# Kernel optimization log

Measured on AMD Instinct MI355X. Metric: run time of the kernel, lower is better.

The kernel has to match this reference:

```python
import jax, jax.numpy as jnp
import numpy as np

GROUP_SIZE = 32
QMIN, QMAX = -128, 127  # int8 activation range


def setup_inputs() -> dict:
    key = jax.random.key(0)
    k1, k2, k3, k4 = jax.random.split(key, 4)
    B, S, IN, OUT = 4, 2048, 4096, 11008
    G = IN // GROUP_SIZE
    x = jax.random.normal(k1, (B, S, IN), dtype=jnp.float32)
    # unpacked uint4 stored as int8, values in [0, 16)
    weight = jax.random.randint(k2, (OUT, IN), 0, 16, dtype=jnp.int8)
    scales = jax.random.uniform(k3, (OUT, G), minval=0.005, maxval=0.02, dtype=jnp.float32)
    zeros = jax.random.randint(k4, (OUT, G), 0, 16).astype(jnp.float32)
    return {"input": x, "weight": weight, "scales": scales, "zeros": zeros}


def reference(input, weight, scales, zeros):
    OUT, IN = weight.shape
    G = IN // GROUP_SIZE
    # groupwise dequant of int4 weights: w_fp = (q - zero) * scale per group
    w = weight.astype(jnp.float32).reshape(OUT, G, GROUP_SIZE)
    w_dq = ((w - zeros[:, :, None]) * scales[:, :, None]).reshape(OUT, IN)
    # dynamic per-token symmetric int8 quantization of the activation
    amax = jnp.max(jnp.abs(input), axis=-1, keepdims=True)  # [B,S,1]
    a_scale = jnp.maximum(amax, 1e-12) / 127.0
    q_act = jnp.clip(jnp.round(input / a_scale), QMIN, QMAX)
    x_dq = q_act * a_scale  # fake-quantized activation, same math as int8 dot * scales
    # fused dequant-matmul: [B,S,IN] x [OUT,IN] -> [B,S,OUT]
    return jnp.einsum('bsi,oi->bso', x_dq, w_dq)
```

## Files before the change

kernel.cpp:

```cpp
#include <hip/hip_runtime.h>
#include <hip/hip_bf16.h>
#include <stdint.h>

#define M_TOK 8192
#define K_IN  4096
#define N_OUT 11008
#define G_CNT 128
#define BM 128
#define BN 256
#define TILES_M 64
#define TILES_N 43

typedef __attribute__((ext_vector_type(4)))  int   int4v;
typedef __attribute__((ext_vector_type(16))) int   int16v;
typedef __attribute__((ext_vector_type(4)))  float floatx4;

__device__ __forceinline__ void gld16(const void* g, void* lds) {
  __builtin_amdgcn_global_load_lds(
      (const __attribute__((address_space(1))) unsigned int*)g,
      (__attribute__((address_space(3))) unsigned int*)lds,
      16, 0, 0);
}

__device__ __forceinline__ int swz(int r) { return (r & 3) ^ ((r >> 2) & 1); }

__global__ void detect_kernel(const int* __restrict__ w, int* __restrict__ flag) {
  int bad = 0;
  int t = threadIdx.x;
  for (int i = t; i < 4096; i += 64) {
    int v = w[i];
    bad |= (v < 0) | (v > 15);
  }
  bad = __any(bad);
  if (t == 0) *flag = bad ? 1 : 0;
}

__global__ __launch_bounds__(256) void wdq8_kernel(
    const int* __restrict__ w, const float* __restrict__ scales,
    const float* __restrict__ zeros, signed char* __restrict__ w8,
    float* __restrict__ wrsc, const int* __restrict__ flag) {
  int n = blockIdx.x;
  int t = threadIdx.x;
  int k0 = t << 4;
  int g  = k0 >> 5;
  float s = scales[(size_t)n * G_CNT + g];
  float z = zeros[(size_t)n * G_CNT + g];
  float wf[16];
  if (*flag == 0) {
    const int4* p = (const int4*)(w + (size_t)n * K_IN + k0);
#pragma unroll
    for (int i = 0; i < 4; ++i) {
      int4 a = p[i];
      wf[4 * i + 0] = ((float)a.x - z) * s;
      wf[4 * i + 1] = ((float)a.y - z) * s;
      wf[4 * i + 2] = ((float)a.z - z) * s;
      wf[4 * i + 3] = ((float)a.w - z) * s;
    }
  } else {
    const unsigned char* wb = (const unsigned char*)w;
    uint4 u = *(const uint4*)(wb + (size_t)n * K_IN + k0);
    unsigned int uu[4] = {u.x, u.y, u.z, u.w};
#pragma unroll
    for (int i = 0; i < 4; ++i)
#pragma unroll
      for (int b = 0; b < 4; ++b)
        wf[4 * i + b] = ((float)((uu[i] >> (8 * b)) & 0xFFu) - z) * s;
  }
  float mx = 0.f;
#pragma unroll
  for (int i = 0; i < 16; ++i) mx = fmaxf(mx, fabsf(wf[i]));
#pragma unroll
  for (int off = 32; off > 0; off >>= 1)
    mx = fmaxf(mx, __shfl_xor(mx, off, 64));
  __shared__ float sm[4];
  if ((t & 63) == 0) sm[t >> 6] = mx;
  __syncthreads();
  mx = fmaxf(fmaxf(sm[0], sm[1]), fmaxf(sm[2], sm[3]));
  mx = fmaxf(mx, 1e-20f);
  if (t == 0) wrsc[n] = mx / 127.f;
  float inv = 127.f / mx;
  unsigned int ob[4];
#pragma unroll
  for (int i = 0; i < 4; ++i) {
    unsigned int v = 0;
#pragma unroll
    for (int b = 0; b < 4; ++b) {
      int q = (int)rintf(wf[4 * i + b] * inv);
      q = q > 127 ? 127 : (q < -127 ? -127 : q);
      v |= ((unsigned int)(q & 0xFF)) << (8 * b);
    }
    ob[i] = v;
  }
  *(uint4*)(w8 + (size_t)n * K_IN + k0) = make_uint4(ob[0], ob[1], ob[2], ob[3]);
}

__global__ __launch_bounds__(256) void act8_kernel(
    const float* __restrict__ x, signed char* __restrict__ aq,
    float* __restrict__ ascale) {
  int row = blockIdx.x;
  const float4* xr = (const float4*)(x + (size_t)row * K_IN);
  int t = threadIdx.x;
  float4 v[4];
  float am = 0.f;
#pragma unroll
  for (int i = 0; i < 4; ++i) {
    v[i] = xr[i * 256 + t];
    am = fmaxf(am, fmaxf(fmaxf(fabsf(v[i].x), fabsf(v[i].y)),
                         fmaxf(fabsf(v[i].z), fabsf(v[i].w))));
  }
#pragma unroll
  for (int off = 32; off > 0; off >>= 1)
    am = fmaxf(am, __shfl_xor(am, off, 64));
  __shared__ float sm[4];
  if ((t & 63) == 0) sm[t >> 6] = am;
  __syncthreads();
  am = fmaxf(fmaxf(sm[0], sm[1]), fmaxf(sm[2], sm[3]));
  float as_ = fmaxf(am, 1e-12f) / 127.f;
  if (t == 0) ascale[row] = as_;
  int* op = (int*)(aq + (size_t)row * K_IN);
#pragma unroll
  for (int i = 0; i < 4; ++i) {
    float qf[4] = {v[i].x, v[i].y, v[i].z, v[i].w};
    unsigned int pk = 0;
#pragma unroll
    for (int b = 0; b < 4; ++b) {
      float q = fminf(fmaxf(rintf(qf[b] / as_), -128.f), 127.f);
      pk |= ((unsigned int)((int)q & 0xFF)) << (8 * b);
    }
    op[i * 256 + t] = (int)pk;
  }
}

__global__ __launch_bounds__(256, 2) void gemm_i8_kernel(
    const signed char* __restrict__ A8,
    const signed char* __restrict__ W8,
    const float* __restrict__ Ascale,
    const float* __restrict__ Wrsc,
    float* __restrict__ C) {
  __shared__ __attribute__((aligned(16))) signed char lA[BM * 64];
  __shared__ __attribute__((aligned(16))) signed char lB[BN * 64];

  int bx = blockIdx.x;
  int band = bx / (8 * TILES_N);
  int rem  = bx % (8 * TILES_N);
  int tm = band * 8 + (rem & 7);
  int tn = rem >> 3;
  int m0 = tm * BM, n0 = tn * BN;

  int t = threadIdx.x;
  int lane = t & 63;
  int w = t >> 6;
  int wm = (w >> 1) * 64, wn = (w & 1) * 128;
  int half = lane >> 5, r31 = lane & 31;

  int lrow = lane >> 2;
  int lchunk = lane & 3;
  const signed char* pA[2];
  const signed char* pB[4];
#pragma unroll
  for (int r = 0; r < 2; ++r) {
    int grow = w * 32 + r * 16 + lrow;
    int scol = (lchunk ^ swz(grow)) << 4;
    pA[r] = A8 + (size_t)(m0 + grow) * K_IN + scol;
  }
#pragma unroll
  for (int r = 0; r < 4; ++r) {
    int grow = w * 64 + r * 16 + lrow;
    int scol = (lchunk ^ swz(grow)) << 4;
    pB[r] = W8 + (size_t)(n0 + grow) * K_IN + scol;
  }

  int aoff[2][2], boff[4][2];
#pragma unroll
  for (int i = 0; i < 2; ++i) {
    int R = wm + i * 32 + r31;
    int sw = swz(R);
#pragma unroll
    for (int ks = 0; ks < 2; ++ks)
      aoff[i][ks] = R * 64 + (((ks * 2 + half) ^ sw) << 4);
  }
#pragma unroll
  for (int j = 0; j < 4; ++j) {
    int R = wn + j * 32 + r31;
    int sw = swz(R);
#pragma unroll
    for (int ks = 0; ks < 2; ++ks)
      boff[j][ks] = R * 64 + (((ks * 2 + half) ^ sw) << 4);
  }

  int16v acc[2][4];
#pragma unroll
  for (int i = 0; i < 2; ++i)
#pragma unroll
    for (int j = 0; j < 4; ++j)
#pragma unroll
      for (int e = 0; e < 16; ++e) acc[i][j][e] = 0;

  char* lAb = (char*)lA;
  char* lBb = (char*)lB;

  for (int k0 = 0; k0 < K_IN; k0 += 64) {
#pragma unroll
    for (int r = 0; r < 2; ++r)
      gld16(pA[r], lAb + (w * 32 + r * 16) * 64);
#pragma unroll
    for (int r = 0; r < 4; ++r)
      gld16(pB[r], lBb + (w * 64 + r * 16) * 64);
#pragma unroll
    for (int r = 0; r < 2; ++r) pA[r] += 64;
#pragma unroll
    for (int r = 0; r < 4; ++r) pB[r] += 64;
    __syncthreads();

#pragma unroll
    for (int ks = 0; ks < 2; ++ks) {
      int4v af[2], bf[4];
#pragma unroll
      for (int i = 0; i < 2; ++i) af[i] = *(const int4v*)(lAb + aoff[i][ks]);
#pragma unroll
      for (int j = 0; j < 4; ++j) bf[j] = *(const int4v*)(lBb + boff[j][ks]);
#pragma unroll
      for (int i = 0; i < 2; ++i)
#pragma unroll
        for (int j = 0; j < 4; ++j)
          acc[i][j] = __builtin_amdgcn_mfma_i32_32x32x32_i8(af[i], bf[j], acc[i][j], 0, 0, 0);
    }
    __syncthreads();
  }

  float wsv[4];
#pragma unroll
  for (int j = 0; j < 4; ++j) wsv[j] = Wrsc[n0 + wn + j * 32 + r31];
#pragma unroll
  for (int i = 0; i < 2; ++i) {
#pragma unroll
    for (int rh = 0; rh < 4; ++rh) {
#pragma unroll
      for (int rl = 0; rl < 4; ++rl) {
        int rg = rh * 4 + rl;
        int gm = m0 + wm + i * 32 + rl + 8 * rh + 4 * half;
        float s = Ascale[gm];
        float* crow = C + (size_t)gm * N_OUT + n0 + wn + r31;
#pragma unroll
        for (int j = 0; j < 4; ++j)
          crow[j * 32] = s * wsv[j] * (float)acc[i][j][rg];
      }
    }
  }
}

extern "C" void kernel_launch(void* const* d_in, const int* in_sizes, int n_in,
                              void* d_out, int out_size, void* d_ws, size_t ws_size,
                              hipStream_t stream) {
  const float* x      = (const float*)d_in[0];
  const int*   wraw   = (const int*)d_in[1];
  const float* scales = (const float*)d_in[2];
  const float* zeros  = (const float*)d_in[3];
  float* out = (float*)d_out;

  char* ws = (char*)d_ws;
  signed char* W8 = (signed char*)ws;
  signed char* A8 = (signed char*)(ws + (size_t)N_OUT * K_IN);
  float* Wrsc   = (float*)(ws + (size_t)N_OUT * K_IN + (size_t)M_TOK * K_IN);
  float* Ascale = Wrsc + N_OUT;
  int* flag = (int*)(Ascale + M_TOK);

  detect_kernel<<<1, 64, 0, stream>>>(wraw, flag);
  wdq8_kernel<<<N_OUT, 256, 0, stream>>>(wraw, scales, zeros, W8, Wrsc, flag);
  act8_kernel<<<M_TOK, 256, 0, stream>>>(x, A8, Ascale);
  gemm_i8_kernel<<<TILES_M * TILES_N, 256, 0, stream>>>(A8, W8, Ascale, Wrsc, out);
}
```

Measured before the change: 1.005 ms.

## Triple-buffer LDS tiles in int8 GEMM with async prefetch and MFMA priority

Replaces the single-buffered LDS load/compute loop with a three-stage ring buffer. Each k-step now issues the global-to-LDS loads two steps ahead and waits only on the older loads with partial vmcnt. It also raises wave priority around the MFMA block so compute gets issued ahead of memory work. This aims to hide global load latency behind MFMA work, at the cost of triple the LDS per block (72KB), which may lower occupancy below the two blocks per CU requested in the launch bounds.

```diff
diff --git a/kernel.cpp b/kernel.cpp
--- a/kernel.cpp
+++ b/kernel.cpp
@@ -10,6 +10,8 @@
 #define BN 256
 #define TILES_M 64
 #define TILES_N 43
+#define KT_CNT 64
+#define BUF_BYTES 24576
 
 typedef __attribute__((ext_vector_type(4)))  int   int4v;
 typedef __attribute__((ext_vector_type(16))) int   int16v;
@@ -137,8 +139,7 @@
     const float* __restrict__ Ascale,
     const float* __restrict__ Wrsc,
     float* __restrict__ C) {
-  __shared__ __attribute__((aligned(16))) signed char lA[BM * 64];
-  __shared__ __attribute__((aligned(16))) signed char lB[BN * 64];
+  __shared__ __attribute__((aligned(16))) signed char ldsbuf[3 * BUF_BYTES];
 
   int bx = blockIdx.x;
   int band = bx / (8 * TILES_N);
@@ -196,10 +197,9 @@
 #pragma unroll
       for (int e = 0; e < 16; ++e) acc[i][j][e] = 0;
 
-  char* lAb = (char*)lA;
-  char* lBb = (char*)lB;
-
-  for (int k0 = 0; k0 < K_IN; k0 += 64) {
+  auto STAGE = [&](int bo) {
+    char* lAb = (char*)ldsbuf + bo;
+    char* lBb = lAb + 8192;
 #pragma unroll
     for (int r = 0; r < 2; ++r)
       gld16(pA[r], lAb + (w * 32 + r * 16) * 64);
@@ -210,8 +210,11 @@
     for (int r = 0; r < 2; ++r) pA[r] += 64;
 #pragma unroll
     for (int r = 0; r < 4; ++r) pB[r] += 64;
-    __syncthreads();
-
+  };
+
+  auto COMPUTE = [&](int bo) {
+    const char* lAb = (const char*)ldsbuf + bo;
+    const char* lBb = lAb + 8192;
 #pragma unroll
     for (int ks = 0; ks < 2; ++ks) {
       int4v af[2], bf[4];
@@ -219,14 +222,44 @@
       for (int i = 0; i < 2; ++i) af[i] = *(const int4v*)(lAb + aoff[i][ks]);
 #pragma unroll
       for (int j = 0; j < 4; ++j) bf[j] = *(const int4v*)(lBb + boff[j][ks]);
+      __builtin_amdgcn_s_setprio(1);
 #pragma unroll
       for (int i = 0; i < 2; ++i)
 #pragma unroll
         for (int j = 0; j < 4; ++j)
           acc[i][j] = __builtin_amdgcn_mfma_i32_32x32x32_i8(af[i], bf[j], acc[i][j], 0, 0, 0);
-    }
-    __syncthreads();
-  }
+      __builtin_amdgcn_s_setprio(0);
+    }
+  };
+
+  STAGE(0);
+  STAGE(BUF_BYTES);
+
+  int curo = 0;
+  int stgo = 2 * BUF_BYTES;
+
+  for (int kt = 0; kt < KT_CNT - 2; ++kt) {
+    STAGE(stgo);
+    asm volatile("s_waitcnt vmcnt(12)" ::: "memory");
+    __builtin_amdgcn_s_barrier();
+    asm volatile("" ::: "memory");
+    COMPUTE(curo);
+    asm volatile("" ::: "memory");
+    __builtin_amdgcn_s_barrier();
+    asm volatile("" ::: "memory");
+    curo = (curo == 2 * BUF_BYTES) ? 0 : curo + BUF_BYTES;
+    stgo = (stgo == 2 * BUF_BYTES) ? 0 : stgo + BUF_BYTES;
+  }
+  asm volatile("s_waitcnt vmcnt(6)" ::: "memory");
+  __builtin_amdgcn_s_barrier();
+  asm volatile("" ::: "memory");
+  COMPUTE(curo);
+  curo = (curo == 2 * BUF_BYTES) ? 0 : curo + BUF_BYTES;
+  asm volatile("" ::: "memory");
+  asm volatile("s_waitcnt vmcnt(0)" ::: "memory");
+  __builtin_amdgcn_s_barrier();
+  asm volatile("" ::: "memory");
+  COMPUTE(curo);
 
   float wsv[4];
 #pragma unroll
```

Result: no change. 992.0 us (-1.3%).

## Enlarge GEMM tile to 256x256 with triple-buffered LDS pipeline

Applied to the files above, without the earlier changes.

Grows the int8 GEMM block tile from 128x256 to 256x256 with 512 threads (8 waves, each computing 128x64), and replaces the load-sync-compute loop with a triple-buffered LDS pipeline. Global-to-LDS loads for later k-tiles are interleaved with MFMA quads under fine-grained barriers and s_setprio. The aim is to hide global load latency and raise data reuse per byte loaded. The cost is 96KB of LDS per block plus many barriers per k-tile, which may limit occupancy to one block per CU despite the launch bound of 2.

```diff
diff --git a/kernel.cpp b/kernel.cpp
--- a/kernel.cpp
+++ b/kernel.cpp
@@ -6,14 +6,16 @@
 #define K_IN  4096
 #define N_OUT 11008
 #define G_CNT 128
-#define BM 128
+#define BM 256
 #define BN 256
-#define TILES_M 64
+#define TILES_M 32
 #define TILES_N 43
+#define KT_CNT 64
+#define ABYTES 16384
+#define BUF_BYTES 32768
 
 typedef __attribute__((ext_vector_type(4)))  int   int4v;
 typedef __attribute__((ext_vector_type(16))) int   int16v;
-typedef __attribute__((ext_vector_type(4)))  float floatx4;
 
 __device__ __forceinline__ void gld16(const void* g, void* lds) {
   __builtin_amdgcn_global_load_lds(
@@ -131,14 +133,13 @@
   }
 }
 
-__global__ __launch_bounds__(256, 2) void gemm_i8_kernel(
+__global__ __launch_bounds__(512, 2) void gemm_i8_kernel(
     const signed char* __restrict__ A8,
     const signed char* __restrict__ W8,
     const float* __restrict__ Ascale,
     const float* __restrict__ Wrsc,
     float* __restrict__ C) {
-  __shared__ __attribute__((aligned(16))) signed char lA[BM * 64];
-  __shared__ __attribute__((aligned(16))) signed char lB[BN * 64];
+  __shared__ __attribute__((aligned(16))) signed char ldsbuf[3 * BUF_BYTES];
 
   int bx = blockIdx.x;
   int band = bx / (8 * TILES_N);
@@ -150,29 +151,27 @@
   int t = threadIdx.x;
   int lane = t & 63;
   int w = t >> 6;
-  int wm = (w >> 1) * 64, wn = (w & 1) * 128;
+  int wm = (w >> 2) * 128;
+  int wn = (w & 3) * 64;
   int half = lane >> 5, r31 = lane & 31;
 
   int lrow = lane >> 2;
   int lchunk = lane & 3;
   const signed char* pA[2];
-  const signed char* pB[4];
+  const signed char* pB[2];
 #pragma unroll
   for (int r = 0; r < 2; ++r) {
     int grow = w * 32 + r * 16 + lrow;
     int scol = (lchunk ^ swz(grow)) << 4;
     pA[r] = A8 + (size_t)(m0 + grow) * K_IN + scol;
-  }
-#pragma unroll
-  for (int r = 0; r < 4; ++r) {
-    int grow = w * 64 + r * 16 + lrow;
-    int scol = (lchunk ^ swz(grow)) << 4;
     pB[r] = W8 + (size_t)(n0 + grow) * K_IN + scol;
   }
-
-  int aoff[2][2], boff[4][2];
-#pragma unroll
-  for (int i = 0; i < 2; ++i) {
+  int sArow0 = (w * 32) * 64;
+  int sArow1 = (w * 32 + 16) * 64;
+
+  int aoff[4][2], boff[2][2];
+#pragma unroll
+  for (int i = 0; i < 4; ++i) {
     int R = wm + i * 32 + r31;
     int sw = swz(R);
 #pragma unroll
@@ -180,7 +179,7 @@
       aoff[i][ks] = R * 64 + (((ks * 2 + half) ^ sw) << 4);
   }
 #pragma unroll
-  for (int j = 0; j < 4; ++j) {
+  for (int j = 0; j < 2; ++j) {
     int R = wn + j * 32 + r31;
     int sw = swz(R);
 #pragma unroll
@@ -188,51 +187,98 @@
       boff[j][ks] = R * 64 + (((ks * 2 + half) ^ sw) << 4);
   }
 
-  int16v acc[2][4];
-#pragma unroll
-  for (int i = 0; i < 2; ++i)
-#pragma unroll
-    for (int j = 0; j < 4; ++j)
+  int16v acc[4][2];
+#pragma unroll
+  for (int i = 0; i < 4; ++i)
+#pragma unroll
+    for (int j = 0; j < 2; ++j)
 #pragma unroll
       for (int e = 0; e < 16; ++e) acc[i][j][e] = 0;
 
-  char* lAb = (char*)lA;
-  char* lBb = (char*)lB;
-
-  for (int k0 = 0; k0 < K_IN; k0 += 64) {
-#pragma unroll
-    for (int r = 0; r < 2; ++r)
-      gld16(pA[r], lAb + (w * 32 + r * 16) * 64);
-#pragma unroll
-    for (int r = 0; r < 4; ++r)
-      gld16(pB[r], lBb + (w * 64 + r * 16) * 64);
-#pragma unroll
-    for (int r = 0; r < 2; ++r) pA[r] += 64;
-#pragma unroll
-    for (int r = 0; r < 4; ++r) pB[r] += 64;
-    __syncthreads();
-
-#pragma unroll
-    for (int ks = 0; ks < 2; ++ks) {
-      int4v af[2], bf[4];
-#pragma unroll
-      for (int i = 0; i < 2; ++i) af[i] = *(const int4v*)(lAb + aoff[i][ks]);
-#pragma unroll
-      for (int j = 0; j < 4; ++j) bf[j] = *(const int4v*)(lBb + boff[j][ks]);
-#pragma unroll
-      for (int i = 0; i < 2; ++i)
-#pragma unroll
-        for (int j = 0; j < 4; ++j)
-          acc[i][j] = __builtin_amdgcn_mfma_i32_32x32x32_i8(af[i], bf[j], acc[i][j], 0, 0, 0);
-    }
-    __syncthreads();
-  }
-
-  float wsv[4];
-#pragma unroll
-  for (int j = 0; j < 4; ++j) wsv[j] = Wrsc[n0 + wn + j * 32 + r31];
-#pragma unroll
-  for (int i = 0; i < 2; ++i) {
+#define MFMA_QUAD(I0, I1, Af0, Af1, Bf0, Bf1)                                   \
+  __builtin_amdgcn_s_setprio(1);                                                \
+  acc[I0][0] = __builtin_amdgcn_mfma_i32_32x32x32_i8(Af0, Bf0, acc[I0][0],0,0,0);\
+  acc[I0][1] = __builtin_amdgcn_mfma_i32_32x32x32_i8(Af0, Bf1, acc[I0][1],0,0,0);\
+  acc[I1][0] = __builtin_amdgcn_mfma_i32_32x32x32_i8(Af1, Bf0, acc[I1][0],0,0,0);\
+  acc[I1][1] = __builtin_amdgcn_mfma_i32_32x32x32_i8(Af1, Bf1, acc[I1][1],0,0,0);\
+  __builtin_amdgcn_s_setprio(0);
+
+#define FENCE asm volatile("" ::: "memory")
+
+#define TILE_BODY(DO_STG, VM_WAIT)                                              \
+  {                                                                             \
+    const char* lAb = (const char*)ldsbuf + curo;                               \
+    const char* lBb = lAb + ABYTES;                                             \
+    char* sAb = (char*)ldsbuf + stgo;                                           \
+    char* sBb = sAb + ABYTES;                                                   \
+    int4v a0, a1, b0, b1;                                                       \
+                        \
+    a0 = *(const int4v*)(lAb + aoff[0][0]);                                     \
+    a1 = *(const int4v*)(lAb + aoff[1][0]);                                     \
+    b0 = *(const int4v*)(lBb + boff[0][0]);                                     \
+    b1 = *(const int4v*)(lBb + boff[1][0]);                                     \
+    if (DO_STG) { gld16(pA[0], sAb + sArow0); pA[0] += 64; }                    \
+    FENCE; __builtin_amdgcn_s_barrier();                                        \
+    MFMA_QUAD(0, 1, a0, a1, b0, b1)                                             \
+    FENCE; __builtin_amdgcn_s_barrier();                                        \
+                                                        \
+    a0 = *(const int4v*)(lAb + aoff[2][0]);                                     \
+    a1 = *(const int4v*)(lAb + aoff[3][0]);                                     \
+    if (DO_STG) { gld16(pA[1], sAb + sArow1); pA[1] += 64; }                    \
+    FENCE; __builtin_amdgcn_s_barrier();                                        \
+    MFMA_QUAD(2, 3, a0, a1, b0, b1)                                             \
+    FENCE; __builtin_amdgcn_s_barrier();                                        \
+                                           \
+    a0 = *(const int4v*)(lAb + aoff[0][1]);                                     \
+    a1 = *(const int4v*)(lAb + aoff[1][1]);                                     \
+    b0 = *(const int4v*)(lBb + boff[0][1]);                                     \
+    b1 = *(const int4v*)(lBb + boff[1][1]);                                     \
+    if (DO_STG) { gld16(pB[0], sBb + sArow0); pB[0] += 64; }                    \
+    FENCE; __builtin_amdgcn_s_barrier();                                        \
+    MFMA_QUAD(0, 1, a0, a1, b0, b1)                                             \
+    FENCE; __builtin_amdgcn_s_barrier();                                        \
+           \
+    a0 = *(const int4v*)(lAb + aoff[2][1]);                                     \
+    a1 = *(const int4v*)(lAb + aoff[3][1]);                                     \
+    if (DO_STG) { gld16(pB[1], sBb + sArow1); pB[1] += 64; }                    \
+    FENCE;                                                                      \
+    VM_WAIT;                                                                    \
+    __builtin_amdgcn_s_barrier();                                               \
+    MFMA_QUAD(2, 3, a0, a1, b0, b1)                                             \
+    FENCE; __builtin_amdgcn_s_barrier();                                        \
+  }
+
+  auto STAGE = [&](int bo) {
+    char* sAb = (char*)ldsbuf + bo;
+    char* sBb = sAb + ABYTES;
+    gld16(pA[0], sAb + sArow0); pA[0] += 64;
+    gld16(pA[1], sAb + sArow1); pA[1] += 64;
+    gld16(pB[0], sBb + sArow0); pB[0] += 64;
+    gld16(pB[1], sBb + sArow1); pB[1] += 64;
+  };
+
+  STAGE(0);
+  STAGE(BUF_BYTES);
+  asm volatile("s_waitcnt vmcnt(4)" ::: "memory");
+  __builtin_amdgcn_s_barrier();
+
+  int curo = 0;
+  int stgo = 2 * BUF_BYTES;
+
+  for (int kt = 0; kt < KT_CNT - 2; ++kt) {
+    TILE_BODY(1, asm volatile("s_waitcnt vmcnt(4)" ::: "memory"))
+    curo = (curo == 2 * BUF_BYTES) ? 0 : curo + BUF_BYTES;
+    stgo = (stgo == 2 * BUF_BYTES) ? 0 : stgo + BUF_BYTES;
+  }
+  TILE_BODY(0, asm volatile("s_waitcnt vmcnt(0)" ::: "memory"))
+  curo = (curo == 2 * BUF_BYTES) ? 0 : curo + BUF_BYTES;
+  TILE_BODY(0, )
+
+  float wsv[2];
+#pragma unroll
+  for (int j = 0; j < 2; ++j) wsv[j] = Wrsc[n0 + wn + j * 32 + r31];
+#pragma unroll
+  for (int i = 0; i < 4; ++i) {
 #pragma unroll
     for (int rh = 0; rh < 4; ++rh) {
 #pragma unroll
@@ -242,11 +288,14 @@
         float s = Ascale[gm];
         float* crow = C + (size_t)gm * N_OUT + n0 + wn + r31;
 #pragma unroll
-        for (int j = 0; j < 4; ++j)
+        for (int j = 0; j < 2; ++j)
           crow[j * 32] = s * wsv[j] * (float)acc[i][j][rg];
       }
     }
   }
+#undef TILE_BODY
+#undef MFMA_QUAD
+#undef FENCE
 }
 
 extern "C" void kernel_launch(void* const* d_in, const int* in_sizes, int n_in,
@@ -268,5 +317,5 @@
   detect_kernel<<<1, 64, 0, stream>>>(wraw, flag);
   wdq8_kernel<<<N_OUT, 256, 0, stream>>>(wraw, scales, zeros, W8, Wrsc, flag);
   act8_kernel<<<M_TOK, 256, 0, stream>>>(x, A8, Ascale);
-  gemm_i8_kernel<<<TILES_M * TILES_N, 256, 0, stream>>>(A8, W8, Ascale, Wrsc, out);
-}
+  gemm_i8_kernel<<<TILES_M * TILES_N, 512, 0, stream>>>(A8, W8, Ascale, Wrsc, out);
+}
```

Result: faster. 945.6 us (-5.9%).
